# Kernel optimization log

Measured on AMD Instinct MI355X. Metric: run time of the kernel, lower is better.

The kernel has to match this reference:

```python
import jax, jax.numpy as jnp
import numpy as np

EPS = 1e-12          # matches torch F.normalize eps
NOW = 3600.0         # fixed 'current time'; timestamps are in [0,1)
TIME_DECAY = 3600.0  # temporal decay constant from the module

def setup_inputs() -> dict:
    key = jax.random.key(0)
    k1, k2, k3, k4, k5 = jax.random.split(key, 5)
    M, D, S = 100000, 768, 2
    return {
        "query_features": jax.random.normal(k1, (D,), dtype=jnp.float32),
        "location": jax.random.normal(k2, (S,), dtype=jnp.float32),
        "memory_features": jax.random.normal(k3, (M, D), dtype=jnp.float32),
        "memory_locations": jax.random.normal(k4, (M, S), dtype=jnp.float32),
        "memory_metadata": jax.random.uniform(k5, (M, 4), dtype=jnp.float32),
        "k": 5,
    }

def reference(query_features, location, memory_features, memory_locations, memory_metadata, k):
    # --- cosine similarity: normalize query and memory rows (F.normalize semantics) ---
    q_norm = query_features / jnp.maximum(jnp.linalg.norm(query_features), EPS)      # [D]
    m_norms = jnp.maximum(jnp.linalg.norm(memory_features, axis=1, keepdims=True), EPS)
    m_norm = memory_features / m_norms                                               # [M, D]
    sim_scores = m_norm @ q_norm                                                     # [M] GEMV

    # --- spatial score: 1 / (1 + euclidean distance to query location) ---
    dists = jnp.linalg.norm(memory_locations - location[None, :], axis=1)            # [M]
    spatial_scores = 1.0 / (1.0 + dists)

    # --- temporal score: exp(-age / 3600) ---
    strengths = memory_metadata[:, 0]
    timestamps = memory_metadata[:, 1]
    ages = NOW - timestamps
    temporal_scores = jnp.exp(-ages / TIME_DECAY)

    combined = (0.5 * sim_scores + 0.3 * spatial_scores + 0.2 * temporal_scores) * strengths

    top_scores, top_indices = jax.lax.top_k(combined, k)
    return top_scores, top_indices
```

## Files before the change

kernel.cpp:

```cpp
#include <hip/hip_runtime.h>
#include <math.h>

#define EPS   1e-12f
#define NOW_T 3600.0f
#define TDEC  3600.0f
#define K     5
#define D     768

__global__ __launch_bounds__(256) void score_kernel(
    const float* __restrict__ q,
    const float* __restrict__ loc,
    const float* __restrict__ feat,
    const float* __restrict__ mloc,
    const float* __restrict__ meta,
    float* __restrict__ scores,
    int M)
{
    const int lane   = threadIdx.x & 63;
    const int wib    = threadIdx.x >> 6;
    const int wpb    = blockDim.x >> 6;
    const int gwave  = blockIdx.x * wpb + wib;
    const int nwaves = gridDim.x * wpb;

    const int c = lane * 4;
    float4 q0 = *(const float4*)(q + c);
    float4 q1 = *(const float4*)(q + c + 256);
    float4 q2 = *(const float4*)(q + c + 512);

    float qss = q0.x*q0.x + q0.y*q0.y + q0.z*q0.z + q0.w*q0.w
              + q1.x*q1.x + q1.y*q1.y + q1.z*q1.z + q1.w*q1.w
              + q2.x*q2.x + q2.y*q2.y + q2.z*q2.z + q2.w*q2.w;
    #pragma unroll
    for (int m = 1; m < 64; m <<= 1) qss += __shfl_xor(qss, m);
    const float inv_qn = 1.0f / fmaxf(sqrtf(qss), EPS);

    const float lx = loc[0];
    const float ly = loc[1];

    for (int row = gwave; row < M; row += nwaves) {
        const float* r = feat + (size_t)row * D;
        float4 f0 = *(const float4*)(r + c);
        float4 f1 = *(const float4*)(r + c + 256);
        float4 f2 = *(const float4*)(r + c + 512);

        float dot = 0.f, ss = 0.f;
        dot = fmaf(f0.x, q0.x, dot); ss = fmaf(f0.x, f0.x, ss);
        dot = fmaf(f0.y, q0.y, dot); ss = fmaf(f0.y, f0.y, ss);
        dot = fmaf(f0.z, q0.z, dot); ss = fmaf(f0.z, f0.z, ss);
        dot = fmaf(f0.w, q0.w, dot); ss = fmaf(f0.w, f0.w, ss);
        dot = fmaf(f1.x, q1.x, dot); ss = fmaf(f1.x, f1.x, ss);
        dot = fmaf(f1.y, q1.y, dot); ss = fmaf(f1.y, f1.y, ss);
        dot = fmaf(f1.z, q1.z, dot); ss = fmaf(f1.z, f1.z, ss);
        dot = fmaf(f1.w, q1.w, dot); ss = fmaf(f1.w, f1.w, ss);
        dot = fmaf(f2.x, q2.x, dot); ss = fmaf(f2.x, f2.x, ss);
        dot = fmaf(f2.y, q2.y, dot); ss = fmaf(f2.y, f2.y, ss);
        dot = fmaf(f2.z, q2.z, dot); ss = fmaf(f2.z, f2.z, ss);
        dot = fmaf(f2.w, q2.w, dot); ss = fmaf(f2.w, f2.w, ss);

        #pragma unroll
        for (int m = 1; m < 64; m <<= 1) {
            dot += __shfl_xor(dot, m);
            ss  += __shfl_xor(ss,  m);
        }

        if (lane == 0) {
            float sim = dot * inv_qn / fmaxf(sqrtf(ss), EPS);
            float2 ml = *(const float2*)(mloc + (size_t)row * 2);
            float4 md = *(const float4*)(meta + (size_t)row * 4);
            float dx = ml.x - lx, dy = ml.y - ly;
            float dist = sqrtf(dx*dx + dy*dy);
            float spatial  = 1.0f / (1.0f + dist);
            float temporal = expf((md.y - NOW_T) / TDEC);
            scores[row] = (0.5f*sim + 0.3f*spatial + 0.2f*temporal) * md.x;
        }
    }
}

__global__ __launch_bounds__(1024) void topk_kernel(
    const float* __restrict__ scores, int M, float* __restrict__ out)
{
    __shared__ float s_val[1024 * K];
    __shared__ int   s_idx[1024 * K];

    const int tid = threadIdx.x;
    float v[K]; int ix[K];
    #pragma unroll
    for (int j = 0; j < K; ++j) { v[j] = -INFINITY; ix[j] = -1; }

    for (int i = tid; i < M; i += blockDim.x) {
        float s = scores[i];
        if (s > v[K-1]) {
            int j = K - 1;
            #pragma unroll
            for (int t = K - 1; t > 0; --t) {
                if (v[t-1] < s) { v[t] = v[t-1]; ix[t] = ix[t-1]; j = t - 1; }
            }
            v[j] = s; ix[j] = i;
        }
    }

    #pragma unroll
    for (int j = 0; j < K; ++j) { s_val[tid*K + j] = v[j]; s_idx[tid*K + j] = ix[j]; }
    __syncthreads();

    for (int sz = blockDim.x >> 1; sz >= 1; sz >>= 1) {
        if (tid < sz) {
            const float* pv = &s_val[(tid + sz) * K];
            const int*   pi = &s_idx[(tid + sz) * K];
            float mv[K]; int mi[K];
            int a = 0, b = 0;
            #pragma unroll
            for (int j = 0; j < K; ++j) {
                bool takeA = (b >= K) || (a < K && v[a] >= pv[b]);
                if (takeA) { mv[j] = v[a];  mi[j] = ix[a]; ++a; }
                else       { mv[j] = pv[b]; mi[j] = pi[b]; ++b; }
            }
            #pragma unroll
            for (int j = 0; j < K; ++j) {
                v[j] = mv[j]; ix[j] = mi[j];
                s_val[tid*K + j] = v[j]; s_idx[tid*K + j] = ix[j];
            }
        }
        __syncthreads();
    }

    if (tid == 0) {
        #pragma unroll
        for (int j = 0; j < K; ++j) {
            out[j]     = v[j];
            out[K + j] = (float)ix[j];
        }
    }
}

extern "C" void kernel_launch(void* const* d_in, const int* in_sizes, int n_in,
                              void* d_out, int out_size, void* d_ws, size_t ws_size,
                              hipStream_t stream) {
    const float* q    = (const float*)d_in[0];
    const float* loc  = (const float*)d_in[1];
    const float* feat = (const float*)d_in[2];
    const float* mloc = (const float*)d_in[3];
    const float* meta = (const float*)d_in[4];
    const int M = in_sizes[2] / D;

    float* scores = (float*)d_ws;

    score_kernel<<<2048, 256, 0, stream>>>(q, loc, feat, mloc, meta, scores, M);
    topk_kernel<<<1, 1024, 0, stream>>>(scores, M, (float*)d_out);
}
```

Measured before the change: 466.8 us.

## Use 16-lane groups per row in score kernel and vectorize top-k scan

The score kernel moves from one 64-lane wave per row in a grid-stride loop to one 16-thread group per row, with one launch covering all rows. Each thread keeps 12 float4 query chunks in registers and reduces with 4 shuffle steps instead of 6. This cuts shuffle-reduction overhead per row and puts more independent loads in flight per thread, at the cost of more registers and many more blocks. The single-block top-k scan now reads scores as float4 to cut load instructions.

```diff
diff --git a/kernel.cpp b/kernel.cpp
--- a/kernel.cpp
+++ b/kernel.cpp
@@ -16,63 +16,65 @@
     float* __restrict__ scores,
     int M)
 {
-    const int lane   = threadIdx.x & 63;
-    const int wib    = threadIdx.x >> 6;
-    const int wpb    = blockDim.x >> 6;
-    const int gwave  = blockIdx.x * wpb + wib;
-    const int nwaves = gridDim.x * wpb;
+    const int tid = threadIdx.x;
+    const int c   = tid & 15;
+    const int g   = tid >> 4;
+    const int row = blockIdx.x * 16 + g;
 
-    const int c = lane * 4;
-    float4 q0 = *(const float4*)(q + c);
-    float4 q1 = *(const float4*)(q + c + 256);
-    float4 q2 = *(const float4*)(q + c + 512);
-
-    float qss = q0.x*q0.x + q0.y*q0.y + q0.z*q0.z + q0.w*q0.w
-              + q1.x*q1.x + q1.y*q1.y + q1.z*q1.z + q1.w*q1.w
-              + q2.x*q2.x + q2.y*q2.y + q2.z*q2.z + q2.w*q2.w;
+    const float* qp = q + c * 4;
+    float4 qv[12];
+    float qss = 0.f;
     #pragma unroll
-    for (int m = 1; m < 64; m <<= 1) qss += __shfl_xor(qss, m);
+    for (int j = 0; j < 12; ++j) {
+        qv[j] = *(const float4*)(qp + j * 64);
+        qss = fmaf(qv[j].x, qv[j].x, qss);
+        qss = fmaf(qv[j].y, qv[j].y, qss);
+        qss = fmaf(qv[j].z, qv[j].z, qss);
+        qss = fmaf(qv[j].w, qv[j].w, qss);
+    }
+    #pragma unroll
+    for (int m = 1; m < 16; m <<= 1) qss += __shfl_xor(qss, m);
     const float inv_qn = 1.0f / fmaxf(sqrtf(qss), EPS);
 
-    const float lx = loc[0];
-    const float ly = loc[1];
+    float dot = 0.f, ss = 0.f;
+    if (row < M) {
+        const float* r = feat + (size_t)row * D + c * 4;
+        #pragma unroll
+        for (int j = 0; j < 12; ++j) {
+            float4 f = *(const float4*)(r + j * 64);
+            dot = fmaf(f.x, qv[j].x, dot); ss = fmaf(f.x, f.x, ss);
+            dot = fmaf(f.y, qv[j].y, dot); ss = fmaf(f.y, f.y, ss);
+            dot = fmaf(f.z, qv[j].z, dot); ss = fmaf(f.z, f.z, ss);
+            dot = fmaf(f.w, qv[j].w, dot); ss = fmaf(f.w, f.w, ss);
+        }
+    }
+    #pragma unroll
+    for (int m = 1; m < 16; m <<= 1) {
+        dot += __shfl_xor(dot, m);
+        ss  += __shfl_xor(ss,  m);
+    }
 
-    for (int row = gwave; row < M; row += nwaves) {
-        const float* r = feat + (size_t)row * D;
-        float4 f0 = *(const float4*)(r + c);
-        float4 f1 = *(const float4*)(r + c + 256);
-        float4 f2 = *(const float4*)(r + c + 512);
+    if (row < M && c == 0) {
+        float sim = dot * inv_qn / fmaxf(sqrtf(ss), EPS);
+        float2 ml = *(const float2*)(mloc + (size_t)row * 2);
+        float4 md = *(const float4*)(meta + (size_t)row * 4);
+        float dx = ml.x - loc[0], dy = ml.y - loc[1];
+        float dist = sqrtf(dx * dx + dy * dy);
+        float spatial  = 1.0f / (1.0f + dist);
+        float temporal = expf((md.y - NOW_T) / TDEC);
+        scores[row] = (0.5f * sim + 0.3f * spatial + 0.2f * temporal) * md.x;
+    }
+}
 
-        float dot = 0.f, ss = 0.f;
-        dot = fmaf(f0.x, q0.x, dot); ss = fmaf(f0.x, f0.x, ss);
-        dot = fmaf(f0.y, q0.y, dot); ss = fmaf(f0.y, f0.y, ss);
-        dot = fmaf(f0.z, q0.z, dot); ss = fmaf(f0.z, f0.z, ss);
-        dot = fmaf(f0.w, q0.w, dot); ss = fmaf(f0.w, f0.w, ss);
-        dot = fmaf(f1.x, q1.x, dot); ss = fmaf(f1.x, f1.x, ss);
-        dot = fmaf(f1.y, q1.y, dot); ss = fmaf(f1.y, f1.y, ss);
-        dot = fmaf(f1.z, q1.z, dot); ss = fmaf(f1.z, f1.z, ss);
-        dot = fmaf(f1.w, q1.w, dot); ss = fmaf(f1.w, f1.w, ss);
-        dot = fmaf(f2.x, q2.x, dot); ss = fmaf(f2.x, f2.x, ss);
-        dot = fmaf(f2.y, q2.y, dot); ss = fmaf(f2.y, f2.y, ss);
-        dot = fmaf(f2.z, q2.z, dot); ss = fmaf(f2.z, f2.z, ss);
-        dot = fmaf(f2.w, q2.w, dot); ss = fmaf(f2.w, f2.w, ss);
-
+__device__ __forceinline__ void consider(float (&v)[K], int (&ix)[K], float s, int i)
+{
+    if (s > v[K - 1]) {
+        int j = K - 1;
         #pragma unroll
-        for (int m = 1; m < 64; m <<= 1) {
-            dot += __shfl_xor(dot, m);
-            ss  += __shfl_xor(ss,  m);
+        for (int t = K - 1; t > 0; --t) {
+            if (v[t - 1] < s) { v[t] = v[t - 1]; ix[t] = ix[t - 1]; j = t - 1; }
         }
-
-        if (lane == 0) {
-            float sim = dot * inv_qn / fmaxf(sqrtf(ss), EPS);
-            float2 ml = *(const float2*)(mloc + (size_t)row * 2);
-            float4 md = *(const float4*)(meta + (size_t)row * 4);
-            float dx = ml.x - lx, dy = ml.y - ly;
-            float dist = sqrtf(dx*dx + dy*dy);
-            float spatial  = 1.0f / (1.0f + dist);
-            float temporal = expf((md.y - NOW_T) / TDEC);
-            scores[row] = (0.5f*sim + 0.3f*spatial + 0.2f*temporal) * md.x;
-        }
+        v[j] = s; ix[j] = i;
     }
 }
 
@@ -87,23 +89,23 @@
     #pragma unroll
     for (int j = 0; j < K; ++j) { v[j] = -INFINITY; ix[j] = -1; }
 
-    for (int i = tid; i < M; i += blockDim.x) {
-        float s = scores[i];
-        if (s > v[K-1]) {
-            int j = K - 1;
-            #pragma unroll
-            for (int t = K - 1; t > 0; --t) {
-                if (v[t-1] < s) { v[t] = v[t-1]; ix[t] = ix[t-1]; j = t - 1; }
-            }
-            v[j] = s; ix[j] = i;
-        }
+    const int M4 = M >> 2;
+    const float4* s4 = (const float4*)scores;
+    for (int i = tid; i < M4; i += 1024) {
+        float4 s = s4[i];
+        consider(v, ix, s.x, 4 * i + 0);
+        consider(v, ix, s.y, 4 * i + 1);
+        consider(v, ix, s.z, 4 * i + 2);
+        consider(v, ix, s.w, 4 * i + 3);
     }
+    for (int i = (M4 << 2) + tid; i < M; i += 1024)
+        consider(v, ix, scores[i], i);
 
     #pragma unroll
-    for (int j = 0; j < K; ++j) { s_val[tid*K + j] = v[j]; s_idx[tid*K + j] = ix[j]; }
+    for (int j = 0; j < K; ++j) { s_val[tid * K + j] = v[j]; s_idx[tid * K + j] = ix[j]; }
     __syncthreads();
 
-    for (int sz = blockDim.x >> 1; sz >= 1; sz >>= 1) {
+    for (int sz = 1024 >> 1; sz >= 1; sz >>= 1) {
         if (tid < sz) {
             const float* pv = &s_val[(tid + sz) * K];
             const int*   pi = &s_idx[(tid + sz) * K];
@@ -118,7 +120,7 @@
             #pragma unroll
             for (int j = 0; j < K; ++j) {
                 v[j] = mv[j]; ix[j] = mi[j];
-                s_val[tid*K + j] = v[j]; s_idx[tid*K + j] = ix[j];
+                s_val[tid * K + j] = v[j]; s_idx[tid * K + j] = ix[j];
             }
         }
         __syncthreads();
@@ -145,6 +147,6 @@
 
     float* scores = (float*)d_ws;
 
-    score_kernel<<<2048, 256, 0, stream>>>(q, loc, feat, mloc, meta, scores, M);
+    score_kernel<<<(M + 15) / 16, 256, 0, stream>>>(q, loc, feat, mloc, meta, scores, M);
     topk_kernel<<<1, 1024, 0, stream>>>(scores, M, (float*)d_out);
 }
```

New measurement: 448.5 us. -3.9%, faster.
